# Performance work log

Hardware: AMD Instinct MI355X
Metric: run time of the kernel (lower is better)

Reference implementation:

```python
import jax, jax.numpy as jnp
import numpy as np

B, N, C, H = 32, 197, 768, 12
D = C // H  # head dim = 64


def setup_inputs() -> dict:
    key = jax.random.key(0)
    ks = jax.random.split(key, 5)
    std = 0.02
    x = jax.random.normal(ks[0], (B, N, C), dtype=jnp.float32)
    w_qkv = jax.random.normal(ks[1], (C, 3 * C), dtype=jnp.float32) * std
    w_proj = jax.random.normal(ks[2], (C, C), dtype=jnp.float32) * std
    b_proj = jnp.zeros((C,), dtype=jnp.float32)
    # 1x1 convs over the head axis of the attention map (Conv2d(H,H,1,bias=False))
    w_conv_l = jax.random.normal(ks[3], (H, H), dtype=jnp.float32) * std + jnp.eye(H, dtype=jnp.float32)
    w_conv_w = jax.random.normal(ks[4], (H, H), dtype=jnp.float32) * std + jnp.eye(H, dtype=jnp.float32)
    return {"x": x, "w_qkv": w_qkv, "w_proj": w_proj, "b_proj": b_proj,
            "w_conv_l": w_conv_l, "w_conv_w": w_conv_w}


def reference(x, w_qkv, w_proj, b_proj, w_conv_l, w_conv_w):
    b, n, c = x.shape
    h, d = H, c // H
    scale = d ** (-0.5)
    qkv = (x @ w_qkv).reshape(b, n, 3, h, d).transpose(2, 0, 3, 1, 4)  # [3,B,H,N,D]
    q, k, v = qkv[0], qkv[1], qkv[2]
    # value_map branch (control_output.need_value_map=True)
    value_map = jax.nn.softmax(jnp.einsum('bhnd,bhmd->bhnm', v, v) * scale, axis=-1)
    # scaled QK^T
    attn = jnp.einsum('bhnd,bhmd->bhnm', q * scale, k)  # [B,H,N,N]
    attention_scores = attn  # need_attn_score=True (captured pre-conv)
    # conv_l: 1x1 conv mixing heads
    attn = jnp.einsum('oh,bhnm->bonm', w_conv_l, attn)
    attention_probs = jax.nn.softmax(attn, axis=-1)  # need_attn_prob=True
    # conv_w: 1x1 conv mixing heads on the probabilities
    attn_w = jnp.einsum('oh,bhnm->bonm', w_conv_w, attention_probs)
    out = jnp.einsum('bhnm,bhmd->bhnd', attn_w, v)  # [B,H,N,D]
    out = out.transpose(0, 2, 1, 3).reshape(b, n, c)
    attention_output = out @ w_proj + b_proj
    return attention_output, attention_scores, attention_probs, value_map
```

## Files before the change

### kernel.cpp

```cpp
#include <hip/hip_runtime.h>
#include <cmath>

#define B_ 32
#define N_ 197
#define C_ 768
#define H_ 12
#define D_ 64
#define M_ (B_*N_)
#define MPAD_ 6400
#define K3_ (3*C_)
#define NN_ (N_*N_)
#define BH_ (B_*H_)
#define NP_ 208
#define KP_ 224
#define SCALE 0.125f

typedef __bf16 bf16x8 __attribute__((ext_vector_type(8)));
typedef __bf16 bf16x4 __attribute__((ext_vector_type(4)));
typedef float  f32x4  __attribute__((ext_vector_type(4)));
typedef float  f32x4u __attribute__((ext_vector_type(4), aligned(4)));

__device__ __forceinline__ void gl_lds16(const void* g, void* l) {
    __builtin_amdgcn_global_load_lds(
        (const __attribute__((address_space(1))) void*)g,
        (__attribute__((address_space(3))) void*)l,
        16, 0, 0);
}

__device__ __forceinline__ void transpose_tile(const float* __restrict__ W,
        __bf16* __restrict__ Wt, int R, int Ccols, int c0, int r0,
        float (*t)[33], int tid) {
    const int tx = tid & 31, ty = tid >> 5;
    #pragma unroll
    for (int i = ty; i < 32; i += 8)
        t[i][tx] = W[(size_t)(r0 + i) * Ccols + c0 + tx];
    __syncthreads();
    #pragma unroll
    for (int i = ty; i < 32; i += 8)
        Wt[(size_t)(c0 + i) * R + r0 + tx] = (__bf16)t[tx][i];
}

__global__ __launch_bounds__(256) void prep_kernel(const float* __restrict__ X,
        __bf16* __restrict__ Xb, const float* __restrict__ Wq,
        __bf16* __restrict__ Wqt, const float* __restrict__ Wp,
        __bf16* __restrict__ Wpt) {
    __shared__ float t[32][33];
    const int bid = blockIdx.x, tid = threadIdx.x;
    if (bid < 4800) {
        const long long i = ((long long)bid * 256 + tid) * 4;
        bf16x4 o;
        if (i < (long long)M_ * 768) {
            float4 f = *(const float4*)&X[i];
            o.x = (__bf16)f.x; o.y = (__bf16)f.y; o.z = (__bf16)f.z; o.w = (__bf16)f.w;
        } else {
            o.x = o.y = o.z = o.w = (__bf16)0.f;
        }
        *(bf16x4*)&Xb[i] = o;
    } else if (bid < 6528) {
        const int tt = bid - 4800;
        transpose_tile(Wq, Wqt, 768, K3_, (tt % 72) * 32, (tt / 72) * 32, t, tid);
    } else {
        const int tt = bid - 6528;
        transpose_tile(Wp, Wpt, 768, 768, (tt % 24) * 32, (tt / 24) * 32, t, tid);
    }
}

__global__ __launch_bounds__(256) void mfma_qkv(const __bf16* __restrict__ Xb,
        const __bf16* __restrict__ Wt, __bf16* __restrict__ q,
        __bf16* __restrict__ k, __bf16* __restrict__ v) {
    __shared__ __bf16 As[128*32];
    __shared__ __bf16 Bs[128*32];
    const int tid = threadIdx.x;
    const int wv = tid >> 6, ln = tid & 63;
    const int R0 = blockIdx.x * 128;
    const int C0 = blockIdx.y * 128;
    const int wm = wv >> 1, wn = wv & 1;
    const int arow = ln >> 2, akg = ln & 3;
    f32x4 acc[4][4] = {};
    for (int k0 = 0; k0 < 768; k0 += 32) {
        __syncthreads();
        #pragma unroll
        for (int s = 0; s < 2; s++) {
            const int seg = wv + s*4;
            const int row = seg*16 + arow;
            gl_lds16(Xb + (size_t)(R0 + row)*768 + k0 + akg*8,
                     (char*)As + seg*1024 + ln*16);
            gl_lds16(Wt + (size_t)(C0 + row)*768 + k0 + akg*8,
                     (char*)Bs + seg*1024 + ln*16);
        }
        __syncthreads();
        bf16x8 af[4], bfr[4];
        #pragma unroll
        for (int t = 0; t < 4; t++) {
            af[t]  = *(const bf16x8*)((const char*)As +
                        (wm*64 + t*16 + (ln & 15))*64 + (ln >> 4)*16);
            bfr[t] = *(const bf16x8*)((const char*)Bs +
                        (wn*64 + t*16 + (ln & 15))*64 + (ln >> 4)*16);
        }
        #pragma unroll
        for (int i = 0; i < 4; i++)
            #pragma unroll
            for (int j = 0; j < 4; j++)
                acc[i][j] = __builtin_amdgcn_mfma_f32_16x16x32_bf16(
                                af[i], bfr[j], acc[i][j], 0, 0, 0);
    }
    const int lr = (ln >> 4) * 4;
    const int lc = ln & 15;
    #pragma unroll
    for (int j = 0; j < 4; j++) {
        const int c = C0 + wn*64 + j*16 + lc;
        const int which = c / 768;
        const int rem = c - which*768;
        const int h = rem >> 6, d = rem & 63;
        __bf16* dst = (which == 0) ? q : ((which == 1) ? k : v);
        #pragma unroll
        for (int i = 0; i < 4; i++) {
            #pragma unroll
            for (int rr = 0; rr < 4; rr++) {
                const int r = R0 + wm*64 + i*16 + lr + rr;
                if (r < M_) {
                    const int bb = r / N_, n = r - bb*N_;
                    dst[(((size_t)(bb*H_ + h))*N_ + n)*64 + d] =
                        (__bf16)acc[i][j][rr];
                }
            }
        }
    }
}

__global__ __launch_bounds__(256) void mfma_proj(const __bf16* __restrict__ Ab,
        const __bf16* __restrict__ Wt, const float* __restrict__ bias,
        float* __restrict__ Y) {
    __shared__ __bf16 As[64*32];
    __shared__ __bf16 Bs[128*32];
    const int tid = threadIdx.x;
    const int wv = tid >> 6, ln = tid & 63;
    const int R0 = blockIdx.x * 64;
    const int C0 = blockIdx.y * 128;
    const int wm = wv >> 1, wn = wv & 1;
    const int arow = ln >> 2, akg = ln & 3;
    f32x4 acc[2][4] = {};
    for (int k0 = 0; k0 < 768; k0 += 32) {
        __syncthreads();
        {
            const int row = wv*16 + arow;
            gl_lds16(Ab + (size_t)(R0 + row)*768 + k0 + akg*8,
                     (char*)As + wv*1024 + ln*16);
        }
        #pragma unroll
        for (int s = 0; s < 2; s++) {
            const int seg = wv + s*4;
            const int row = seg*16 + arow;
            gl_lds16(Wt + (size_t)(C0 + row)*768 + k0 + akg*8,
                     (char*)Bs + seg*1024 + ln*16);
        }
        __syncthreads();
        bf16x8 af[2], bfr[4];
        #pragma unroll
        for (int t = 0; t < 2; t++)
            af[t]  = *(const bf16x8*)((const char*)As +
                        (wm*32 + t*16 + (ln & 15))*64 + (ln >> 4)*16);
        #pragma unroll
        for (int t = 0; t < 4; t++)
            bfr[t] = *(const bf16x8*)((const char*)Bs +
                        (wn*64 + t*16 + (ln & 15))*64 + (ln >> 4)*16);
        #pragma unroll
        for (int i = 0; i < 2; i++)
            #pragma unroll
            for (int j = 0; j < 4; j++)
                acc[i][j] = __builtin_amdgcn_mfma_f32_16x16x32_bf16(
                                af[i], bfr[j], acc[i][j], 0, 0, 0);
    }
    const int lr = (ln >> 4) * 4;
    const int lc = ln & 15;
    #pragma unroll
    for (int j = 0; j < 4; j++) {
        const int c = C0 + wn*64 + j*16 + lc;
        const float bv = bias[c];
        #pragma unroll
        for (int i = 0; i < 2; i++) {
            #pragma unroll
            for (int rr = 0; rr < 4; rr++) {
                const int r = R0 + wm*32 + i*16 + lr + rr;
                if (r < M_) Y[(size_t)r*768 + c] = acc[i][j][rr] + bv;
            }
        }
    }
}

__global__ __launch_bounds__(256) void qkt_vvt(const __bf16* __restrict__ Q,
        const __bf16* __restrict__ Km, const __bf16* __restrict__ V,
        float* __restrict__ S, float* __restrict__ VM) {
    __shared__ __bf16 Al[NP_*64];
    __shared__ __bf16 Bl[NP_*64];
    const int tid = threadIdx.x;
    const int w = tid >> 6, L = tid & 63;
    const int lm = L & 15, lg = L >> 4;
    if (blockIdx.x < BH_) {
        const int bh = blockIdx.x;
        const __bf16* Qb = Q  + (size_t)bh*N_*D_;
        const __bf16* Kb = Km + (size_t)bh*N_*D_;
        for (int i = tid*8; i < NP_*64; i += 2048) {
            const int row = i >> 6;
            bf16x8 z = {};
            *(bf16x8*)&Al[i] = (row < N_) ? *(const bf16x8*)&Qb[i] : z;
            *(bf16x8*)&Bl[i] = (row < N_) ? *(const bf16x8*)&Kb[i] : z;
        }
        __syncthreads();
        for (int nt = w; nt < 13; nt += 4) {
            const bf16x8 q0 = *(const bf16x8*)&Al[(nt*16+lm)*64 + lg*8];
            const bf16x8 q1 = *(const bf16x8*)&Al[(nt*16+lm)*64 + 32 + lg*8];
            const int n = nt*16 + lm;
            float* Srow = S + ((size_t)bh*N_ + n)*N_;
            for (int mt = 0; mt < 13; mt++) {
                const bf16x8 k0 = *(const bf16x8*)&Bl[(mt*16+lm)*64 + lg*8];
                const bf16x8 k1 = *(const bf16x8*)&Bl[(mt*16+lm)*64 + 32 + lg*8];
                f32x4 acc = {};
                acc = __builtin_amdgcn_mfma_f32_16x16x32_bf16(k0, q0, acc, 0, 0, 0);
                acc = __builtin_amdgcn_mfma_f32_16x16x32_bf16(k1, q1, acc, 0, 0, 0);
                if (n < N_) {
                    const int m0 = mt*16 + lg*4;
                    if (m0 + 3 < N_) {
                        f32x4 st;
                        #pragma unroll
                        for (int r = 0; r < 4; r++) st[r] = acc[r] * SCALE;
                        *(f32x4u*)&Srow[m0] = st;
                    } else {
                        #pragma unroll
                        for (int r = 0; r < 4; r++)
                            if (m0 + r < N_) Srow[m0 + r] = acc[r] * SCALE;
                    }
                }
            }
        }
    } else {
        const int bh = blockIdx.x - BH_;
        const __bf16* Vb = V + (size_t)bh*N_*D_;
        for (int i = tid*8; i < NP_*64; i += 2048) {
            const int row = i >> 6;
            bf16x8 z = {};
            *(bf16x8*)&Al[i] = (row < N_) ? *(const bf16x8*)&Vb[i] : z;
        }
        __syncthreads();
        for (int nt = w; nt < 13; nt += 4) {
            const bf16x8 q0 = *(const bf16x8*)&Al[(nt*16+lm)*64 + lg*8];
            const bf16x8 q1 = *(const bf16x8*)&Al[(nt*16+lm)*64 + 32 + lg*8];
            f32x4 acc[13];
            for (int mt = 0; mt < 13; mt++) {
                const bf16x8 a0 = *(const bf16x8*)&Al[(mt*16+lm)*64 + lg*8];
                const bf16x8 a1 = *(const bf16x8*)&Al[(mt*16+lm)*64 + 32 + lg*8];
                f32x4 a = {};
                a = __builtin_amdgcn_mfma_f32_16x16x32_bf16(a0, q0, a, 0, 0, 0);
                a = __builtin_amdgcn_mfma_f32_16x16x32_bf16(a1, q1, a, 0, 0, 0);
                acc[mt] = a;
            }
            #pragma unroll
            for (int mt = 0; mt < 13; mt++)
                #pragma unroll
                for (int r = 0; r < 4; r++) acc[mt][r] *= SCALE;
            #pragma unroll
            for (int r = 0; r < 4; r++)
                if (192 + lg*4 + r >= N_) acc[12][r] = -1e30f;
            float mx = -1e30f;
            #pragma unroll
            for (int mt = 0; mt < 13; mt++)
                #pragma unroll
                for (int r = 0; r < 4; r++) mx = fmaxf(mx, acc[mt][r]);
            mx = fmaxf(mx, __shfl_xor(mx, 16));
            mx = fmaxf(mx, __shfl_xor(mx, 32));
            float sm = 0.f;
            #pragma unroll
            for (int mt = 0; mt < 13; mt++)
                #pragma unroll
                for (int r = 0; r < 4; r++) {
                    const float e = __expf(acc[mt][r] - mx);
                    acc[mt][r] = e;
                    sm += e;
                }
            sm += __shfl_xor(sm, 16);
            sm += __shfl_xor(sm, 32);
            const float inv = 1.f / sm;
            const int n = nt*16 + lm;
            if (n < N_) {
                float* Vrow = VM + ((size_t)bh*N_ + n)*N_;
                #pragma unroll
                for (int mt = 0; mt < 12; mt++) {
                    f32x4 st;
                    #pragma unroll
                    for (int r = 0; r < 4; r++) st[r] = acc[mt][r] * inv;
                    *(f32x4u*)&Vrow[mt*16 + lg*4] = st;
                }
                #pragma unroll
                for (int r = 0; r < 4; r++) {
                    const int m = 192 + lg*4 + r;
                    if (m < N_) Vrow[m] = acc[12][r] * inv;
                }
            }
        }
    }
}

__global__ __launch_bounds__(256) void convl_convw(const float* __restrict__ SC,
        const float* __restrict__ wl, const float* __restrict__ ww,
        float* __restrict__ PR, __bf16* __restrict__ AW) {
    __shared__ float sbuf[12][4][200];
    __shared__ float wls[144];
    __shared__ float wws[144];
    const int tid = threadIdx.x;
    const int b = blockIdx.x / 50;
    const int n0 = (blockIdx.x - b * 50) * 4;
    if (tid < 144) { wls[tid] = wl[tid]; wws[tid] = ww[tid]; }
    for (int i = tid; i < 12*4*200; i += 256) {
        const int h = i / 800, rem = i - h*800, n = rem / 200, m = rem - n*200;
        float vv = 0.f;
        if (m < N_ && n0 + n < N_)
            vv = SC[(((size_t)(b*12 + h))*N_ + n0 + n)*N_ + m];
        sbuf[h][n][m] = vv;
    }
    __syncthreads();
    for (int p = tid; p < 4*N_; p += 256) {
        const int n = p / N_, m = p - n*N_;
        float in[12];
        #pragma unroll
        for (int h = 0; h < 12; h++) in[h] = sbuf[h][n][m];
        #pragma unroll
        for (int o = 0; o < 12; o++) {
            float s = 0.f;
            #pragma unroll
            for (int h = 0; h < 12; h++) s += wls[o*12 + h] * in[h];
            sbuf[o][n][m] = s;
        }
    }
    __syncthreads();
    const int w = tid >> 6, l = tid & 63;
    for (int rid = w; rid < 48; rid += 4) {
        const int o = rid >> 2, n = rid & 3;
        const int ng = n0 + n;
        float vv[4];
        float mx = -1e30f;
        #pragma unroll
        for (int c = 0; c < 4; c++) {
            const int m = l + 64*c;
            vv[c] = (m < N_) ? sbuf[o][n][m] : -1e30f;
            mx = fmaxf(mx, vv[c]);
        }
        #pragma unroll
        for (int off = 32; off; off >>= 1) mx = fmaxf(mx, __shfl_xor(mx, off));
        float s = 0.f;
        #pragma unroll
        for (int c = 0; c < 4; c++) {
            const int m = l + 64*c;
            if (m < N_) { vv[c] = __expf(vv[c] - mx); s += vv[c]; }
        }
        #pragma unroll
        for (int off = 32; off; off >>= 1) s += __shfl_xor(s, off);
        const float inv = 1.f / s;
        #pragma unroll
        for (int c = 0; c < 4; c++) {
            const int m = l + 64*c;
            if (m < N_) {
                const float pv = vv[c] * inv;
                if (ng < N_)
                    PR[((((size_t)(b*12 + o))*N_ + ng)*N_) + m] = pv;
                sbuf[o][n][m] = pv;
            }
        }
    }
    __syncthreads();
    for (int p = tid; p < 4*N_; p += 256) {
        const int n = p / N_, m = p - n*N_;
        const int ng = n0 + n;
        if (ng >= N_) continue;
        float in[12];
        #pragma unroll
        for (int h = 0; h < 12; h++) in[h] = sbuf[h][n][m];
        #pragma unroll
        for (int o = 0; o < 12; o++) {
            float s = 0.f;
            #pragma unroll
            for (int h = 0; h < 12; h++) s += wws[o*12 + h] * in[h];
            AW[((size_t)(b*12 + o)*N_ + ng)*KP_ + m] = (__bf16)s;
        }
    }
    for (int p = tid; p < 12*4*(KP_-N_); p += 256) {
        const int o = p / (4*(KP_-N_));
        const int rem = p - o*(4*(KP_-N_));
        const int n = rem / (KP_-N_);
        const int m = N_ + rem - n*(KP_-N_);
        const int ng = n0 + n;
        if (ng < N_)
            AW[((size_t)(b*12 + o)*N_ + ng)*KP_ + m] = (__bf16)0.f;
    }
}

__global__ __launch_bounds__(256) void av_mfma(const __bf16* __restrict__ AW,
        const __bf16* __restrict__ V, __bf16* __restrict__ OP) {
    __shared__ __bf16 Vt[64*KP_];
    const int tid = threadIdx.x, bh = blockIdx.x;
    const int w = tid >> 6, L = tid & 63;
    for (int i = tid*8; i < 64*KP_; i += 2048) {
        bf16x8 z = {};
        *(bf16x8*)&Vt[i] = z;
    }
    __syncthreads();
    const __bf16* Vb = V + (size_t)bh*N_*D_;
    for (int i = tid*8; i < N_*D_; i += 2048) {
        const int row = i >> 6, col = i & 63;
        const bf16x8 vv = *(const bf16x8*)&Vb[i];
        #pragma unroll
        for (int j = 0; j < 8; j++) Vt[(col+j)*KP_ + row] = vv[j];
    }
    __syncthreads();
    const int lm = L & 15, lg = L >> 4;
    const int b = bh / H_, h = bh - b*H_;
    const __bf16* Ab = AW + (size_t)bh*N_*KP_;
    for (int rt = w; rt < 13; rt += 4) {
        int ar = rt*16 + lm;
        if (ar >= N_) ar = 0;
        f32x4 acc[4] = {};
        #pragma unroll
        for (int k0 = 0; k0 < KP_; k0 += 32) {
            const bf16x8 a = *(const bf16x8*)&Ab[(size_t)ar*KP_ + k0 + lg*8];
            #pragma unroll
            for (int ct = 0; ct < 4; ct++) {
                const bf16x8 bf = *(const bf16x8*)&Vt[(ct*16+lm)*KP_ + k0 + lg*8];
                acc[ct] = __builtin_amdgcn_mfma_f32_16x16x32_bf16(
                              a, bf, acc[ct], 0, 0, 0);
            }
        }
        const int rbase = rt*16 + lg*4;
        #pragma unroll
        for (int ct = 0; ct < 4; ct++) {
            const int d = ct*16 + lm;
            #pragma unroll
            for (int r = 0; r < 4; r++) {
                const int row = rbase + r;
                if (row < N_)
                    OP[((size_t)(b*N_ + row))*C_ + h*64 + d] = (__bf16)acc[ct][r];
            }
        }
    }
}

extern "C" void kernel_launch(void* const* d_in, const int* in_sizes, int n_in,
                              void* d_out, int out_size, void* d_ws, size_t ws_size,
                              hipStream_t stream) {
    const float* x      = (const float*)d_in[0];
    const float* w_qkv  = (const float*)d_in[1];
    const float* w_proj = (const float*)d_in[2];
    const float* b_proj = (const float*)d_in[3];
    const float* w_cl   = (const float*)d_in[4];
    const float* w_cw   = (const float*)d_in[5];

    float* out    = (float*)d_out;
    float* scores = out    + (size_t)M_ * C_;
    float* probs  = scores + (size_t)BH_ * NN_;
    float* vmap   = probs  + (size_t)BH_ * NN_;

    char* base = (char*)d_ws;
    const size_t QS = (size_t)BH_ * N_ * D_;
    __bf16* q   = (__bf16*)base;
    __bf16* k   = q + QS;
    __bf16* v   = k + QS;
    __bf16* Xb  = v + QS;
    __bf16* OPb = Xb;
    __bf16* Wqt = Xb + (size_t)MPAD_*768;
    __bf16* Wpt = Wqt + (size_t)K3_*768;
    __bf16* aw  = Wpt + (size_t)768*768;

    prep_kernel   <<<7104,          256, 0, stream>>>(x, Xb, w_qkv, Wqt, w_proj, Wpt);
    mfma_qkv      <<<dim3(50, 18),  256, 0, stream>>>(Xb, Wqt, q, k, v);
    qkt_vvt       <<<2*BH_,         256, 0, stream>>>(q, k, v, scores, vmap);
    convl_convw   <<<32*50,         256, 0, stream>>>(scores, w_cl, w_cw, probs, aw);
    av_mfma       <<<BH_,           256, 0, stream>>>(aw, v, OPb);
    mfma_proj     <<<dim3(100, 6),  256, 0, stream>>>(OPb, Wpt, b_proj, out);
}
```

Measured before the change: 397.9 us.

## Emit swizzled transposed V from QKV GEMM, XOR-swizzle LDS, split AV blocks

The QKV GEMM epilogue now also writes V in a transposed, XOR-swizzled layout, zero-filled in the prep kernel. This lets av_mfma load it into LDS with direct global-to-LDS copies instead of a scalar in-kernel transpose, and av_mfma is split into two blocks per head to double the grid. The QK^T/VV^T kernels use an XOR swizzle on the LDS tiles to reduce bank conflicts, and the projection GEMM moves to 128-row tiles. The costs are extra scattered global writes in the QKV epilogue, a larger workspace, and V being loaded twice per head in av_mfma.

```diff
diff --git a/kernel.cpp b/kernel.cpp
--- a/kernel.cpp
+++ b/kernel.cpp
@@ -13,6 +13,7 @@
 #define BH_ (B_*H_)
 #define NP_ 208
 #define KP_ 224
+#define VTS_ 256
 #define SCALE 0.125f
 
 typedef __bf16 bf16x8 __attribute__((ext_vector_type(8)));
@@ -43,7 +44,7 @@
 __global__ __launch_bounds__(256) void prep_kernel(const float* __restrict__ X,
         __bf16* __restrict__ Xb, const float* __restrict__ Wq,
         __bf16* __restrict__ Wqt, const float* __restrict__ Wp,
-        __bf16* __restrict__ Wpt) {
+        __bf16* __restrict__ Wpt, __bf16* __restrict__ vT) {
     __shared__ float t[32][33];
     const int bid = blockIdx.x, tid = threadIdx.x;
     if (bid < 4800) {
@@ -59,15 +60,20 @@
     } else if (bid < 6528) {
         const int tt = bid - 4800;
         transpose_tile(Wq, Wqt, 768, K3_, (tt % 72) * 32, (tt / 72) * 32, t, tid);
-    } else {
+    } else if (bid < 7104) {
         const int tt = bid - 6528;
         transpose_tile(Wp, Wpt, 768, 768, (tt % 24) * 32, (tt / 24) * 32, t, tid);
+    } else {
+        const size_t idx = ((size_t)(bid - 7104) * 256 + tid) * 8;
+        bf16x8 z = {};
+        *(bf16x8*)&vT[idx] = z;
     }
 }
 
 __global__ __launch_bounds__(256) void mfma_qkv(const __bf16* __restrict__ Xb,
         const __bf16* __restrict__ Wt, __bf16* __restrict__ q,
-        __bf16* __restrict__ k, __bf16* __restrict__ v) {
+        __bf16* __restrict__ k, __bf16* __restrict__ v,
+        __bf16* __restrict__ vT) {
     __shared__ __bf16 As[128*32];
     __shared__ __bf16 Bs[128*32];
     const int tid = threadIdx.x;
@@ -120,8 +126,12 @@
                 const int r = R0 + wm*64 + i*16 + lr + rr;
                 if (r < M_) {
                     const int bb = r / N_, n = r - bb*N_;
-                    dst[(((size_t)(bb*H_ + h))*N_ + n)*64 + d] =
-                        (__bf16)acc[i][j][rr];
+                    const __bf16 val = (__bf16)acc[i][j][rr];
+                    dst[(((size_t)(bb*H_ + h))*N_ + n)*64 + d] = val;
+                    if (which == 2) {
+                        vT[(((size_t)(bb*H_ + h))*64 + d)*VTS_ +
+                           ((((n >> 3) ^ (d & 7))) << 3) + (n & 7)] = val;
+                    }
                 }
             }
         }
@@ -131,41 +141,37 @@
 __global__ __launch_bounds__(256) void mfma_proj(const __bf16* __restrict__ Ab,
         const __bf16* __restrict__ Wt, const float* __restrict__ bias,
         float* __restrict__ Y) {
-    __shared__ __bf16 As[64*32];
+    __shared__ __bf16 As[128*32];
     __shared__ __bf16 Bs[128*32];
     const int tid = threadIdx.x;
     const int wv = tid >> 6, ln = tid & 63;
-    const int R0 = blockIdx.x * 64;
+    const int R0 = blockIdx.x * 128;
     const int C0 = blockIdx.y * 128;
     const int wm = wv >> 1, wn = wv & 1;
     const int arow = ln >> 2, akg = ln & 3;
-    f32x4 acc[2][4] = {};
+    f32x4 acc[4][4] = {};
     for (int k0 = 0; k0 < 768; k0 += 32) {
         __syncthreads();
-        {
-            const int row = wv*16 + arow;
-            gl_lds16(Ab + (size_t)(R0 + row)*768 + k0 + akg*8,
-                     (char*)As + wv*1024 + ln*16);
-        }
         #pragma unroll
         for (int s = 0; s < 2; s++) {
             const int seg = wv + s*4;
             const int row = seg*16 + arow;
+            gl_lds16(Ab + (size_t)(R0 + row)*768 + k0 + akg*8,
+                     (char*)As + seg*1024 + ln*16);
             gl_lds16(Wt + (size_t)(C0 + row)*768 + k0 + akg*8,
                      (char*)Bs + seg*1024 + ln*16);
         }
         __syncthreads();
-        bf16x8 af[2], bfr[4];
-        #pragma unroll
-        for (int t = 0; t < 2; t++)
+        bf16x8 af[4], bfr[4];
+        #pragma unroll
+        for (int t = 0; t < 4; t++) {
             af[t]  = *(const bf16x8*)((const char*)As +
-                        (wm*32 + t*16 + (ln & 15))*64 + (ln >> 4)*16);
-        #pragma unroll
-        for (int t = 0; t < 4; t++)
+                        (wm*64 + t*16 + (ln & 15))*64 + (ln >> 4)*16);
             bfr[t] = *(const bf16x8*)((const char*)Bs +
                         (wn*64 + t*16 + (ln & 15))*64 + (ln >> 4)*16);
-        #pragma unroll
-        for (int i = 0; i < 2; i++)
+        }
+        #pragma unroll
+        for (int i = 0; i < 4; i++)
             #pragma unroll
             for (int j = 0; j < 4; j++)
                 acc[i][j] = __builtin_amdgcn_mfma_f32_16x16x32_bf16(
@@ -178,10 +184,10 @@
         const int c = C0 + wn*64 + j*16 + lc;
         const float bv = bias[c];
         #pragma unroll
-        for (int i = 0; i < 2; i++) {
+        for (int i = 0; i < 4; i++) {
             #pragma unroll
             for (int rr = 0; rr < 4; rr++) {
-                const int r = R0 + wm*32 + i*16 + lr + rr;
+                const int r = R0 + wm*64 + i*16 + lr + rr;
                 if (r < M_) Y[(size_t)r*768 + c] = acc[i][j][rr] + bv;
             }
         }
@@ -202,19 +208,23 @@
         const __bf16* Kb = Km + (size_t)bh*N_*D_;
         for (int i = tid*8; i < NP_*64; i += 2048) {
             const int row = i >> 6;
+            const int c8 = (i >> 3) & 7;
+            const int di = (i & ~63) | ((c8 ^ (row & 7)) << 3);
             bf16x8 z = {};
-            *(bf16x8*)&Al[i] = (row < N_) ? *(const bf16x8*)&Qb[i] : z;
-            *(bf16x8*)&Bl[i] = (row < N_) ? *(const bf16x8*)&Kb[i] : z;
+            *(bf16x8*)&Al[di] = (row < N_) ? *(const bf16x8*)&Qb[i] : z;
+            *(bf16x8*)&Bl[di] = (row < N_) ? *(const bf16x8*)&Kb[i] : z;
         }
         __syncthreads();
         for (int nt = w; nt < 13; nt += 4) {
-            const bf16x8 q0 = *(const bf16x8*)&Al[(nt*16+lm)*64 + lg*8];
-            const bf16x8 q1 = *(const bf16x8*)&Al[(nt*16+lm)*64 + 32 + lg*8];
-            const int n = nt*16 + lm;
+            const int qr = nt*16 + lm;
+            const bf16x8 q0 = *(const bf16x8*)&Al[qr*64 + ((lg ^ (qr&7)) << 3)];
+            const bf16x8 q1 = *(const bf16x8*)&Al[qr*64 + (((4+lg) ^ (qr&7)) << 3)];
+            const int n = qr;
             float* Srow = S + ((size_t)bh*N_ + n)*N_;
             for (int mt = 0; mt < 13; mt++) {
-                const bf16x8 k0 = *(const bf16x8*)&Bl[(mt*16+lm)*64 + lg*8];
-                const bf16x8 k1 = *(const bf16x8*)&Bl[(mt*16+lm)*64 + 32 + lg*8];
+                const int kr = mt*16 + lm;
+                const bf16x8 k0 = *(const bf16x8*)&Bl[kr*64 + ((lg ^ (kr&7)) << 3)];
+                const bf16x8 k1 = *(const bf16x8*)&Bl[kr*64 + (((4+lg) ^ (kr&7)) << 3)];
                 f32x4 acc = {};
                 acc = __builtin_amdgcn_mfma_f32_16x16x32_bf16(k0, q0, acc, 0, 0, 0);
                 acc = __builtin_amdgcn_mfma_f32_16x16x32_bf16(k1, q1, acc, 0, 0, 0);
@@ -238,17 +248,21 @@
         const __bf16* Vb = V + (size_t)bh*N_*D_;
         for (int i = tid*8; i < NP_*64; i += 2048) {
             const int row = i >> 6;
+            const int c8 = (i >> 3) & 7;
+            const int di = (i & ~63) | ((c8 ^ (row & 7)) << 3);
             bf16x8 z = {};
-            *(bf16x8*)&Al[i] = (row < N_) ? *(const bf16x8*)&Vb[i] : z;
+            *(bf16x8*)&Al[di] = (row < N_) ? *(const bf16x8*)&Vb[i] : z;
         }
         __syncthreads();
         for (int nt = w; nt < 13; nt += 4) {
-            const bf16x8 q0 = *(const bf16x8*)&Al[(nt*16+lm)*64 + lg*8];
-            const bf16x8 q1 = *(const bf16x8*)&Al[(nt*16+lm)*64 + 32 + lg*8];
+            const int qr = nt*16 + lm;
+            const bf16x8 q0 = *(const bf16x8*)&Al[qr*64 + ((lg ^ (qr&7)) << 3)];
+            const bf16x8 q1 = *(const bf16x8*)&Al[qr*64 + (((4+lg) ^ (qr&7)) << 3)];
             f32x4 acc[13];
             for (int mt = 0; mt < 13; mt++) {
-                const bf16x8 a0 = *(const bf16x8*)&Al[(mt*16+lm)*64 + lg*8];
-                const bf16x8 a1 = *(const bf16x8*)&Al[(mt*16+lm)*64 + 32 + lg*8];
+                const int kr = mt*16 + lm;
+                const bf16x8 a0 = *(const bf16x8*)&Al[kr*64 + ((lg ^ (kr&7)) << 3)];
+                const bf16x8 a1 = *(const bf16x8*)&Al[kr*64 + (((4+lg) ^ (kr&7)) << 3)];
                 f32x4 a = {};
                 a = __builtin_amdgcn_mfma_f32_16x16x32_bf16(a0, q0, a, 0, 0, 0);
                 a = __builtin_amdgcn_mfma_f32_16x16x32_bf16(a1, q1, a, 0, 0, 0);
@@ -280,7 +294,7 @@
             sm += __shfl_xor(sm, 16);
             sm += __shfl_xor(sm, 32);
             const float inv = 1.f / sm;
-            const int n = nt*16 + lm;
+            const int n = qr;
             if (n < N_) {
                 float* Vrow = VM + ((size_t)bh*N_ + n)*N_;
                 #pragma unroll
@@ -394,27 +408,22 @@
 }
 
 __global__ __launch_bounds__(256) void av_mfma(const __bf16* __restrict__ AW,
-        const __bf16* __restrict__ V, __bf16* __restrict__ OP) {
-    __shared__ __bf16 Vt[64*KP_];
-    const int tid = threadIdx.x, bh = blockIdx.x;
+        const __bf16* __restrict__ VT, __bf16* __restrict__ OP) {
+    __shared__ __bf16 Vt[64*VTS_];
+    const int tid = threadIdx.x;
+    const int bh = blockIdx.x >> 1, half = blockIdx.x & 1;
     const int w = tid >> 6, L = tid & 63;
-    for (int i = tid*8; i < 64*KP_; i += 2048) {
-        bf16x8 z = {};
-        *(bf16x8*)&Vt[i] = z;
-    }
-    __syncthreads();
-    const __bf16* Vb = V + (size_t)bh*N_*D_;
-    for (int i = tid*8; i < N_*D_; i += 2048) {
-        const int row = i >> 6, col = i & 63;
-        const bf16x8 vv = *(const bf16x8*)&Vb[i];
-        #pragma unroll
-        for (int j = 0; j < 8; j++) Vt[(col+j)*KP_ + row] = vv[j];
-    }
+    const __bf16* Vg = VT + (size_t)bh*64*VTS_;
+    #pragma unroll
+    for (int i = tid; i < 2048; i += 256)
+        gl_lds16(Vg + (size_t)i*8, (char*)Vt + (size_t)i*16);
     __syncthreads();
     const int lm = L & 15, lg = L >> 4;
     const int b = bh / H_, h = bh - b*H_;
     const __bf16* Ab = AW + (size_t)bh*N_*KP_;
-    for (int rt = w; rt < 13; rt += 4) {
+    const int rt0 = half ? 7 : 0;
+    const int rt1 = half ? 13 : 7;
+    for (int rt = rt0 + w; rt < rt1; rt += 4) {
         int ar = rt*16 + lm;
         if (ar >= N_) ar = 0;
         f32x4 acc[4] = {};
@@ -423,7 +432,10 @@
             const bf16x8 a = *(const bf16x8*)&Ab[(size_t)ar*KP_ + k0 + lg*8];
             #pragma unroll
             for (int ct = 0; ct < 4; ct++) {
-                const bf16x8 bf = *(const bf16x8*)&Vt[(ct*16+lm)*KP_ + k0 + lg*8];
+                const int dr = ct*16 + lm;
+                const int slot = (k0 >> 3) + lg;
+                const bf16x8 bf = *(const bf16x8*)
+                    &Vt[dr*VTS_ + ((slot ^ (dr & 7)) << 3)];
                 acc[ct] = __builtin_amdgcn_mfma_f32_16x16x32_bf16(
                               a, bf, acc[ct], 0, 0, 0);
             }
@@ -467,11 +479,13 @@
     __bf16* Wqt = Xb + (size_t)MPAD_*768;
     __bf16* Wpt = Wqt + (size_t)K3_*768;
     __bf16* aw  = Wpt + (size_t)768*768;
-
-    prep_kernel   <<<7104,          256, 0, stream>>>(x, Xb, w_qkv, Wqt, w_proj, Wpt);
-    mfma_qkv      <<<dim3(50, 18),  256, 0, stream>>>(Xb, Wqt, q, k, v);
+    __bf16* vT  = aw  + (size_t)BH_*N_*KP_;
+
+    prep_kernel   <<<10176,         256, 0, stream>>>(x, Xb, w_qkv, Wqt,
+                                                      w_proj, Wpt, vT);
+    mfma_qkv      <<<dim3(50, 18),  256, 0, stream>>>(Xb, Wqt, q, k, v, vT);
     qkt_vvt       <<<2*BH_,         256, 0, stream>>>(q, k, v, scores, vmap);
     convl_convw   <<<32*50,         256, 0, stream>>>(scores, w_cl, w_cw, probs, aw);
-    av_mfma       <<<BH_,           256, 0, stream>>>(aw, v, OPb);
-    mfma_proj     <<<dim3(100, 6),  256, 0, stream>>>(OPb, Wpt, b_proj, out);
-}
+    av_mfma       <<<2*BH_,         256, 0, stream>>>(aw, vT, OPb);
+    mfma_proj     <<<dim3(50, 6),   256, 0, stream>>>(OPb, Wpt, b_proj, out);
+}
```

Result: slower. 413.6 us (+3.9%).
